# Kernel optimization log

Hardware: AMD Instinct MI355X
Metric: run time of the kernel (lower is better)

## Reference

```python
import jax, jax.numpy as jnp
import numpy as np

INPUT_SIZE = 2048
OUTPUT_SIZE = 2048
BATCH = 8192


def setup_inputs() -> dict:
    key = jax.random.key(0)
    ks = jax.random.split(key, 11)
    in_dim = INPUT_SIZE + OUTPUT_SIZE
    bound = 1.0 / np.sqrt(in_dim)  # torch nn.Linear default init range
    def lin(kw, kb):
        W = jax.random.uniform(kw, (OUTPUT_SIZE, in_dim), jnp.float32, -bound, bound)
        b = jax.random.uniform(kb, (OUTPUT_SIZE,), jnp.float32, -bound, bound)
        return W, b
    W1, b1 = lin(ks[0], ks[1])
    W2, b2 = lin(ks[2], ks[3])
    W3, b3 = lin(ks[4], ks[5])
    W4, b4 = lin(ks[6], ks[7])
    i = jax.random.normal(ks[8], (BATCH, INPUT_SIZE), jnp.float32)
    h = jax.random.normal(ks[9], (BATCH, OUTPUT_SIZE), jnp.float32)
    c = jax.random.normal(ks[10], (BATCH, OUTPUT_SIZE), jnp.float32)
    return {"i": i, "h": h, "c": c,
            "W1": W1, "b1": b1, "W2": W2, "b2": b2,
            "W3": W3, "b3": b3, "W4": W4, "b4": b4}


def reference(i, h, c, W1, b1, W2, b2, W3, b3, W4, b4):
    ih = jnp.concatenate((i, h), axis=1)  # [B, input+output]
    o1 = jax.nn.sigmoid(ih @ W1.T + b1)   # forget gate
    o2 = jax.nn.sigmoid(ih @ W2.T + b2)   # input gate
    o3 = jnp.tanh(ih @ W3.T + b3)         # candidate
    o4 = jax.nn.sigmoid(ih @ W4.T + b4)   # output gate
    new_c = c * o1 + o2 * o3
    # NOTE: faithful to the source: new_h uses tanh of the OLD cell state c
    new_h = jnp.tanh(c) * o4
    return (new_h, new_c)
```

## Files before the change

### kernel.cpp

```cpp
#include <hip/hip_runtime.h>
#include <hip/hip_bf16.h>
#include <stdint.h>

#define GLOBAL_AS __attribute__((address_space(1)))
#define LDS_AS    __attribute__((address_space(3)))

typedef __attribute__((ext_vector_type(8))) short  short8;
typedef __attribute__((ext_vector_type(4))) float  floatx4;

constexpr int BATCH = 8192;
constexpr int OUT   = 2048;
constexpr int KDIM  = 4096;

constexpr size_t IH_ELEMS = (size_t)BATCH * KDIM;
constexpr size_t W_ELEMS  = (size_t)4 * OUT * KDIM;

constexpr int TBM = 256;
constexpr int TBN = 256;
constexpr int TBK = 64;
constexpr int TNT = KDIM / TBK;

__device__ __forceinline__ unsigned int cvt2(float a, float b) {
    union { __hip_bfloat162 h; unsigned int u; } v;
    v.h = __float22bfloat162_rn(make_float2(a, b));
    return v.u;
}
__device__ __forceinline__ float sigmoidf_(float x) {
    return 1.0f / (1.0f + __expf(-x));
}
__device__ __forceinline__ void stage16(const unsigned short* g, unsigned short* l) {
    __builtin_amdgcn_global_load_lds((const GLOBAL_AS uint32_t*)g,
                                     (LDS_AS uint32_t*)l, 16, 0, 0);
}
__device__ __forceinline__ floatx4 mfma16(short8 a, short8 b, floatx4 c) {
    return __builtin_amdgcn_mfma_f32_16x16x32_bf16(a, b, c, 0, 0, 0);
}


__global__ __launch_bounds__(256)
void cvt_all(const float* __restrict__ I, const float* __restrict__ H,
             const float* __restrict__ W1, const float* __restrict__ W2,
             const float* __restrict__ W3, const float* __restrict__ W4,
             unsigned short* __restrict__ dst)
{
    const size_t t = (size_t)blockIdx.x * 256 + threadIdx.x;
    const size_t e = t * 8;
    const float* s;
    if (e < IH_ELEMS) {
        const int b = (int)(e >> 12);
        const int k = (int)(e & 4095);
        s = (k < 2048) ? (I + (size_t)b * 2048 + k)
                       : (H + (size_t)b * 2048 + (k - 2048));
    } else {
        const size_t e2 = e - IH_ELEMS;
        const int g = (int)(e2 >> 23);
        const size_t rem = e2 & 8388607u;
        const float* Wg = (g == 0) ? W1 : (g == 1) ? W2 : (g == 2) ? W3 : W4;
        s = Wg + rem;
    }
    const float4 x = ((const float4*)s)[0];
    const float4 y = ((const float4*)s)[1];
    uint4 o;
    o.x = cvt2(x.x, x.y); o.y = cvt2(x.z, x.w);
    o.z = cvt2(y.x, y.y); o.w = cvt2(y.z, y.w);
    *(uint4*)(dst + e) = o;
}


__global__ __launch_bounds__(512, 2)
void lstm_gemm_8ph(const unsigned short* __restrict__ ihb,
                   const unsigned short* __restrict__ Wb,
                   const float* __restrict__ C,
                   const float* __restrict__ B1, const float* __restrict__ B2,
                   const float* __restrict__ B3, const float* __restrict__ B4,
                   float* __restrict__ Outp)
{
    __shared__ unsigned short smem[65536];

    const int tid  = threadIdx.x;
    const int w    = tid >> 6;
    const int lane = tid & 63;
    const int col  = lane & 15;
    const int q    = lane >> 4;
    const int wr   = w >> 2;
    const int wc   = w & 3;

    const int bid = blockIdx.x;
    const int swz = (bid & 7) * 128 + (bid >> 3);
    const int bx  = swz & 31;
    const int by  = swz >> 5;
    const int bm0 = by * TBM;
    const int o0  = bx * 64;

    const unsigned short* srcA[2];
    const unsigned short* srcB[2];
    #pragma unroll
    for (int j = 0; j < 2; ++j) {
        const int c  = (w * 2 + j) * 64 + lane;
        const int r  = c >> 3;
        const int s  = c & 7;
        const int kc = s ^ (r & 7);
        srcA[j] = ihb + (size_t)(bm0 + r) * KDIM + kc * 8;
        const int g  = (r >> 4) & 3;
        const int oo = o0 + (r >> 6) * 16 + (r & 15);
        srcB[j] = Wb + (size_t)(g * OUT + oo) * KDIM + kc * 8;
    }
    const int sliceA = w * 1024;

    const int c7    = col & 7;
    const int slot0 = ((0 + q) ^ c7) * 8;
    const int slot1 = ((4 + q) ^ c7) * 8;
    const int aBase = wr * 8192 + col * 64;
    const int bBase = 16384 + (wc >> 1) * 8192 + ((wc & 1) * 64 + col) * 64;

    floatx4 acc[8][4];
    #pragma unroll
    for (int i = 0; i < 8; ++i)
        #pragma unroll
        for (int j = 0; j < 4; ++j)
            acc[i][j] = (floatx4){0.f, 0.f, 0.f, 0.f};

    stage16(srcA[0],                  &smem[0     + sliceA]);
    stage16(srcA[1],                  &smem[0     + sliceA + 512]);
    stage16(srcA[0] + 128 * KDIM,     &smem[8192  + sliceA]);
    stage16(srcA[1] + 128 * KDIM,     &smem[8192  + sliceA + 512]);
    stage16(srcB[0],                  &smem[16384 + sliceA]);
    stage16(srcB[1],                  &smem[16384 + sliceA + 512]);
    stage16(srcB[0] + 32 * KDIM,      &smem[24576 + sliceA]);
    stage16(srcB[1] + 32 * KDIM,      &smem[24576 + sliceA + 512]);
    stage16(srcB[0] + TBK,            &smem[32768 + 16384 + sliceA]);
    stage16(srcB[1] + TBK,            &smem[32768 + 16384 + sliceA + 512]);
    stage16(srcB[0] + 32 * KDIM + TBK, &smem[32768 + 24576 + sliceA]);
    stage16(srcB[1] + 32 * KDIM + TBK, &smem[32768 + 24576 + sliceA + 512]);
    asm volatile("s_waitcnt vmcnt(4)" ::: "memory");
    __builtin_amdgcn_s_barrier();

    short8 Af[4][2];
    short8 Bf[2][2][2];

    for (int t = 0; t < TNT; ++t) {
        const int buf = t & 1;
        const unsigned short* Ab = smem + buf * 32768 + aBase;
        const unsigned short* Bb = smem + buf * 32768 + bBase;
        unsigned short* stA = smem + (buf ^ 1) * 32768;
        unsigned short* stB = smem + buf * 32768;
        const int kA = ((t + 1) < TNT ? (t + 1) : TNT - 1) * TBK;
        const int kB = ((t + 2) < TNT ? (t + 2) : TNT - 1) * TBK;

        #pragma unroll
        for (int tm = 0; tm < 4; ++tm) {
            Af[tm][0] = *(const short8*)(Ab + tm * 1024 + slot0);
            Af[tm][1] = *(const short8*)(Ab + tm * 1024 + slot1);
        }
        #pragma unroll
        for (int tn = 0; tn < 2; ++tn) {
            Bf[0][tn][0] = *(const short8*)(Bb + tn * 1024 + slot0);
            Bf[0][tn][1] = *(const short8*)(Bb + tn * 1024 + slot1);
        }
        stage16(srcA[0] + kA, stA + 0 + sliceA);
        stage16(srcA[1] + kA, stA + 0 + sliceA + 512);
        __builtin_amdgcn_s_barrier();
        asm volatile("s_waitcnt lgkmcnt(0)" ::: "memory");
        __builtin_amdgcn_sched_barrier(0);
        __builtin_amdgcn_s_setprio(1);
        #pragma unroll
        for (int tm = 0; tm < 4; ++tm)
            #pragma unroll
            for (int tn = 0; tn < 2; ++tn) {
                acc[tm][tn] = mfma16(Af[tm][0], Bf[0][tn][0], acc[tm][tn]);
                acc[tm][tn] = mfma16(Af[tm][1], Bf[0][tn][1], acc[tm][tn]);
            }
        __builtin_amdgcn_s_setprio(0);
        __builtin_amdgcn_s_barrier();

        #pragma unroll
        for (int tn = 0; tn < 2; ++tn) {
            Bf[1][tn][0] = *(const short8*)(Bb + 2048 + tn * 1024 + slot0);
            Bf[1][tn][1] = *(const short8*)(Bb + 2048 + tn * 1024 + slot1);
        }
        stage16(srcA[0] + 128 * KDIM + kA, stA + 8192 + sliceA);
        stage16(srcA[1] + 128 * KDIM + kA, stA + 8192 + sliceA + 512);
        __builtin_amdgcn_s_barrier();
        asm volatile("s_waitcnt lgkmcnt(0)" ::: "memory");
        __builtin_amdgcn_sched_barrier(0);
        __builtin_amdgcn_s_setprio(1);
        #pragma unroll
        for (int tm = 0; tm < 4; ++tm)
            #pragma unroll
            for (int tn = 0; tn < 2; ++tn) {
                acc[tm][2 + tn] = mfma16(Af[tm][0], Bf[1][tn][0], acc[tm][2 + tn]);
                acc[tm][2 + tn] = mfma16(Af[tm][1], Bf[1][tn][1], acc[tm][2 + tn]);
            }
        __builtin_amdgcn_s_setprio(0);
        __builtin_amdgcn_s_barrier();

        #pragma unroll
        for (int tm = 0; tm < 4; ++tm) {
            Af[tm][0] = *(const short8*)(Ab + 4096 + tm * 1024 + slot0);
            Af[tm][1] = *(const short8*)(Ab + 4096 + tm * 1024 + slot1);
        }
        stage16(srcB[0] + kB, stB + 16384 + sliceA);
        stage16(srcB[1] + kB, stB + 16384 + sliceA + 512);
        __builtin_amdgcn_s_barrier();
        asm volatile("s_waitcnt lgkmcnt(0)" ::: "memory");
        __builtin_amdgcn_sched_barrier(0);
        __builtin_amdgcn_s_setprio(1);
        #pragma unroll
        for (int tm = 0; tm < 4; ++tm)
            #pragma unroll
            for (int tn = 0; tn < 2; ++tn) {
                acc[4 + tm][tn] = mfma16(Af[tm][0], Bf[0][tn][0], acc[4 + tm][tn]);
                acc[4 + tm][tn] = mfma16(Af[tm][1], Bf[0][tn][1], acc[4 + tm][tn]);
            }
        __builtin_amdgcn_s_setprio(0);
        __builtin_amdgcn_s_barrier();

        stage16(srcB[0] + 32 * KDIM + kB, stB + 24576 + sliceA);
        stage16(srcB[1] + 32 * KDIM + kB, stB + 24576 + sliceA + 512);
        __builtin_amdgcn_s_barrier();
        asm volatile("s_waitcnt lgkmcnt(0)" ::: "memory");
        __builtin_amdgcn_sched_barrier(0);
        __builtin_amdgcn_s_setprio(1);
        #pragma unroll
        for (int tm = 0; tm < 4; ++tm)
            #pragma unroll
            for (int tn = 0; tn < 2; ++tn) {
                acc[4 + tm][2 + tn] = mfma16(Af[tm][0], Bf[1][tn][0], acc[4 + tm][2 + tn]);
                acc[4 + tm][2 + tn] = mfma16(Af[tm][1], Bf[1][tn][1], acc[4 + tm][2 + tn]);
            }
        __builtin_amdgcn_s_setprio(0);
        asm volatile("s_waitcnt vmcnt(4)" ::: "memory");
        __builtin_amdgcn_s_barrier();
    }

    const int o = o0 + wc * 16 + col;
    float bias[4];
    bias[0] = B1[o]; bias[1] = B2[o]; bias[2] = B3[o]; bias[3] = B4[o];

    const size_t HALF = (size_t)BATCH * OUT;
    #pragma unroll
    for (int tm = 0; tm < 8; ++tm) {
        #pragma unroll
        for (int r = 0; r < 4; ++r) {
            const int b = bm0 + wr * 128 + tm * 16 + q * 4 + r;
            const size_t idx = (size_t)b * OUT + o;
            const float cv = C[idx];
            const float o1 = sigmoidf_(acc[tm][0][r] + bias[0]);
            const float o2 = sigmoidf_(acc[tm][1][r] + bias[1]);
            const float o3 = tanhf    (acc[tm][2][r] + bias[2]);
            const float o4 = sigmoidf_(acc[tm][3][r] + bias[3]);
            Outp[idx]        = tanhf(cv) * o4;
            Outp[HALF + idx] = cv * o1 + o2 * o3;
        }
    }
}


constexpr int FBM = 128;
constexpr int FBO = 32;
constexpr int FBK = 32;

__global__ __launch_bounds__(256)
void lstm_fused_f32(const float* __restrict__ I, const float* __restrict__ H,
                    const float* __restrict__ C,
                    const float* __restrict__ W1, const float* __restrict__ B1,
                    const float* __restrict__ W2, const float* __restrict__ B2,
                    const float* __restrict__ W3, const float* __restrict__ B3,
                    const float* __restrict__ W4, const float* __restrict__ B4,
                    float* __restrict__ Outp)
{
    __shared__ unsigned short As[FBM * FBK];
    __shared__ unsigned short Bs[4 * FBO * FBK];

    const int tid  = threadIdx.x;
    const int w    = tid >> 6;
    const int lane = tid & 63;
    const int col  = lane & 15;
    const int q    = lane >> 4;

    const int bm0 = blockIdx.y * FBM;
    const int o0  = blockIdx.x * FBO;

    long aoff[2], boff[2];
    const float* wptr[2];
    unsigned short* dstA[2];
    unsigned short* dstB[2];
    #pragma unroll
    for (int j = 0; j < 2; ++j) {
        const int win = w * 2 + j;
        const int c   = win * 64 + lane;
        const int row = c >> 2;
        const int kcs = c & 3;
        const int kc  = kcs ^ ((row >> 1) & 3);
        aoff[j] = (long)(bm0 + row) * (KDIM / 2) + kc * 8;
        const int g = row >> 5;
        const int o = o0 + (row & 31);
        wptr[j] = (g == 0) ? W1 : (g == 1) ? W2 : (g == 2) ? W3 : W4;
        boff[j] = (long)o * KDIM + kc * 8;
        dstA[j] = As + (size_t)c * 8;
        dstB[j] = Bs + (size_t)c * 8;
    }

    int aAddr[2];
    #pragma unroll
    for (int tm = 0; tm < 2; ++tm) {
        const int m = w * 32 + tm * 16 + col;
        aAddr[tm] = (m * 4 + (q ^ ((m >> 1) & 3))) * 8;
    }
    int bAddr[8];
    #pragma unroll
    for (int tn = 0; tn < 8; ++tn) {
        const int n = tn * 16 + col;
        bAddr[tn] = (n * 4 + (q ^ ((n >> 1) & 3))) * 8;
    }

    floatx4 acc[2][8];
    #pragma unroll
    for (int tm = 0; tm < 2; ++tm)
        #pragma unroll
        for (int tn = 0; tn < 8; ++tn)
            acc[tm][tn] = (floatx4){0.f, 0.f, 0.f, 0.f};

    for (int k0 = 0; k0 < KDIM; k0 += FBK) {
        #pragma unroll
        for (int j = 0; j < 2; ++j) {
            const float* ab = (k0 < KDIM / 2) ? (I + k0) : (H + (k0 - KDIM / 2));
            const float* sa = ab + aoff[j];
            const float* sb = wptr[j] + boff[j] + k0;
            const float4 a0 = ((const float4*)sa)[0];
            const float4 a1 = ((const float4*)sa)[1];
            const float4 b0 = ((const float4*)sb)[0];
            const float4 b1 = ((const float4*)sb)[1];
            uint4 va, vb;
            va.x = cvt2(a0.x, a0.y); va.y = cvt2(a0.z, a0.w);
            va.z = cvt2(a1.x, a1.y); va.w = cvt2(a1.z, a1.w);
            vb.x = cvt2(b0.x, b0.y); vb.y = cvt2(b0.z, b0.w);
            vb.z = cvt2(b1.x, b1.y); vb.w = cvt2(b1.z, b1.w);
            *(uint4*)dstA[j] = va;
            *(uint4*)dstB[j] = vb;
        }
        __syncthreads();

        const short8 a0 = *(const short8*)(As + aAddr[0]);
        const short8 a1 = *(const short8*)(As + aAddr[1]);
        #pragma unroll
        for (int tn = 0; tn < 8; ++tn) {
            const short8 b = *(const short8*)(Bs + bAddr[tn]);
            acc[0][tn] = __builtin_amdgcn_mfma_f32_16x16x32_bf16(a0, b, acc[0][tn], 0, 0, 0);
            acc[1][tn] = __builtin_amdgcn_mfma_f32_16x16x32_bf16(a1, b, acc[1][tn], 0, 0, 0);
        }
        __syncthreads();
    }

    float bias[2][4];
    #pragma unroll
    for (int obit = 0; obit < 2; ++obit) {
        const int o = o0 + obit * 16 + col;
        bias[obit][0] = B1[o]; bias[obit][1] = B2[o];
        bias[obit][2] = B3[o]; bias[obit][3] = B4[o];
    }

    const size_t HALF = (size_t)BATCH * OUT;
    #pragma unroll
    for (int tm = 0; tm < 2; ++tm) {
        #pragma unroll
        for (int r = 0; r < 4; ++r) {
            const int b = bm0 + w * 32 + tm * 16 + q * 4 + r;
            #pragma unroll
            for (int obit = 0; obit < 2; ++obit) {
                const int o = o0 + obit * 16 + col;
                const size_t idx = (size_t)b * OUT + o;
                const float cv = C[idx];
                const float o1 = sigmoidf_(acc[tm][0 + obit][r] + bias[obit][0]);
                const float o2 = sigmoidf_(acc[tm][2 + obit][r] + bias[obit][1]);
                const float o3 = tanhf   (acc[tm][4 + obit][r] + bias[obit][2]);
                const float o4 = sigmoidf_(acc[tm][6 + obit][r] + bias[obit][3]);
                Outp[idx]        = tanhf(cv) * o4;
                Outp[HALF + idx] = cv * o1 + o2 * o3;
            }
        }
    }
}

extern "C" void kernel_launch(void* const* d_in, const int* in_sizes, int n_in,
                              void* d_out, int out_size, void* d_ws, size_t ws_size,
                              hipStream_t stream) {
    const float* I  = (const float*)d_in[0];
    const float* H  = (const float*)d_in[1];
    const float* C  = (const float*)d_in[2];
    const float* W1 = (const float*)d_in[3];
    const float* B1 = (const float*)d_in[4];
    const float* W2 = (const float*)d_in[5];
    const float* B2 = (const float*)d_in[6];
    const float* W3 = (const float*)d_in[7];
    const float* B3 = (const float*)d_in[8];
    const float* W4 = (const float*)d_in[9];
    const float* B4 = (const float*)d_in[10];
    float* Outp = (float*)d_out;

    const size_t need = (IH_ELEMS + W_ELEMS) * 2;

    if (ws_size >= need) {
        unsigned short* ihb = (unsigned short*)d_ws;
        unsigned short* Wb  = ihb + IH_ELEMS;
        const int cvt_blocks = (int)((IH_ELEMS + W_ELEMS) / 8 / 256);
        cvt_all<<<cvt_blocks, 256, 0, stream>>>(I, H, W1, W2, W3, W4, ihb);
        lstm_gemm_8ph<<<dim3((BATCH / TBM) * (OUT / (TBN / 4))), dim3(512), 0, stream>>>(
            ihb, Wb, C, B1, B2, B3, B4, Outp);
    } else {
        dim3 grid(OUT / FBO, BATCH / FBM);
        lstm_fused_f32<<<grid, 256, 0, stream>>>(I, H, C, W1, B1, W2, B2,
                                                 W3, B3, W4, B4, Outp);
    }
}
```

Baseline: 837.1 us.

## Software-pipeline LDS fragment loads one phase ahead of MFMA clusters

Restructures the main K loop so each MFMA cluster consumes fragments loaded during the previous phase. A second A-fragment register set lets the second half's A data and the next tile's A/B fragments be prefetched from LDS while the current MFMAs run. Global-to-LDS staging moves to after the MFMA clusters, and the explicit lgkmcnt(0) waits before each cluster are removed. This raises register pressure and reshuffles barriers and vmcnt waits, which risks LDS race hazards or a loss of occupancy.

Measured after the change: 841.7 us. Within noise of the previous version (+0.6%).

```diff
diff --git a/kernel.cpp b/kernel.cpp
--- a/kernel.cpp
+++ b/kernel.cpp
@@ -120,47 +120,57 @@
         for (int j = 0; j < 4; ++j)
             acc[i][j] = (floatx4){0.f, 0.f, 0.f, 0.f};
 
-    stage16(srcA[0],                  &smem[0     + sliceA]);
-    stage16(srcA[1],                  &smem[0     + sliceA + 512]);
-    stage16(srcA[0] + 128 * KDIM,     &smem[8192  + sliceA]);
-    stage16(srcA[1] + 128 * KDIM,     &smem[8192  + sliceA + 512]);
-    stage16(srcB[0],                  &smem[16384 + sliceA]);
-    stage16(srcB[1],                  &smem[16384 + sliceA + 512]);
-    stage16(srcB[0] + 32 * KDIM,      &smem[24576 + sliceA]);
-    stage16(srcB[1] + 32 * KDIM,      &smem[24576 + sliceA + 512]);
-    stage16(srcB[0] + TBK,            &smem[32768 + 16384 + sliceA]);
-    stage16(srcB[1] + TBK,            &smem[32768 + 16384 + sliceA + 512]);
+    stage16(srcA[0],                   &smem[0     + sliceA]);
+    stage16(srcA[1],                   &smem[0     + sliceA + 512]);
+    stage16(srcA[0] + 128 * KDIM,      &smem[8192  + sliceA]);
+    stage16(srcA[1] + 128 * KDIM,      &smem[8192  + sliceA + 512]);
+    stage16(srcB[0],                   &smem[16384 + sliceA]);
+    stage16(srcB[1],                   &smem[16384 + sliceA + 512]);
+    stage16(srcB[0] + 32 * KDIM,       &smem[24576 + sliceA]);
+    stage16(srcB[1] + 32 * KDIM,       &smem[24576 + sliceA + 512]);
+    stage16(srcB[0] + TBK,             &smem[32768 + 16384 + sliceA]);
+    stage16(srcB[1] + TBK,             &smem[32768 + 16384 + sliceA + 512]);
     stage16(srcB[0] + 32 * KDIM + TBK, &smem[32768 + 24576 + sliceA]);
     stage16(srcB[1] + 32 * KDIM + TBK, &smem[32768 + 24576 + sliceA + 512]);
     asm volatile("s_waitcnt vmcnt(4)" ::: "memory");
     __builtin_amdgcn_s_barrier();
 
     short8 Af[4][2];
+    short8 Af2[4][2];
     short8 Bf[2][2][2];
+
+    {
+        const unsigned short* Ab0 = smem + aBase;
+        const unsigned short* Bb0 = smem + bBase;
+        #pragma unroll
+        for (int tm = 0; tm < 4; ++tm) {
+            Af[tm][0] = *(const short8*)(Ab0 + tm * 1024 + slot0);
+            Af[tm][1] = *(const short8*)(Ab0 + tm * 1024 + slot1);
+        }
+        #pragma unroll
+        for (int tn = 0; tn < 2; ++tn) {
+            Bf[0][tn][0] = *(const short8*)(Bb0 + tn * 1024 + slot0);
+            Bf[0][tn][1] = *(const short8*)(Bb0 + tn * 1024 + slot1);
+        }
+    }
 
     for (int t = 0; t < TNT; ++t) {
         const int buf = t & 1;
-        const unsigned short* Ab = smem + buf * 32768 + aBase;
-        const unsigned short* Bb = smem + buf * 32768 + bBase;
+        const unsigned short* Ab  = smem + buf * 32768 + aBase;
+        const unsigned short* Bb  = smem + buf * 32768 + bBase;
+        const unsigned short* Abn = smem + (buf ^ 1) * 32768 + aBase;
+        const unsigned short* Bbn = smem + (buf ^ 1) * 32768 + bBase;
         unsigned short* stA = smem + (buf ^ 1) * 32768;
         unsigned short* stB = smem + buf * 32768;
         const int kA = ((t + 1) < TNT ? (t + 1) : TNT - 1) * TBK;
         const int kB = ((t + 2) < TNT ? (t + 2) : TNT - 1) * TBK;
 
-        #pragma unroll
-        for (int tm = 0; tm < 4; ++tm) {
-            Af[tm][0] = *(const short8*)(Ab + tm * 1024 + slot0);
-            Af[tm][1] = *(const short8*)(Ab + tm * 1024 + slot1);
-        }
+        __builtin_amdgcn_s_barrier();
         #pragma unroll
         for (int tn = 0; tn < 2; ++tn) {
-            Bf[0][tn][0] = *(const short8*)(Bb + tn * 1024 + slot0);
-            Bf[0][tn][1] = *(const short8*)(Bb + tn * 1024 + slot1);
-        }
-        stage16(srcA[0] + kA, stA + 0 + sliceA);
-        stage16(srcA[1] + kA, stA + 0 + sliceA + 512);
-        __builtin_amdgcn_s_barrier();
-        asm volatile("s_waitcnt lgkmcnt(0)" ::: "memory");
+            Bf[1][tn][0] = *(const short8*)(Bb + 2048 + tn * 1024 + slot0);
+            Bf[1][tn][1] = *(const short8*)(Bb + 2048 + tn * 1024 + slot1);
+        }
         __builtin_amdgcn_sched_barrier(0);
         __builtin_amdgcn_s_setprio(1);
         #pragma unroll
@@ -171,17 +181,17 @@
                 acc[tm][tn] = mfma16(Af[tm][1], Bf[0][tn][1], acc[tm][tn]);
             }
         __builtin_amdgcn_s_setprio(0);
-        __builtin_amdgcn_s_barrier();
-
-        #pragma unroll
-        for (int tn = 0; tn < 2; ++tn) {
-            Bf[1][tn][0] = *(const short8*)(Bb + 2048 + tn * 1024 + slot0);
-            Bf[1][tn][1] = *(const short8*)(Bb + 2048 + tn * 1024 + slot1);
-        }
+        stage16(srcA[0] + kA,             stA + 0    + sliceA);
+        stage16(srcA[1] + kA,             stA + 0    + sliceA + 512);
         stage16(srcA[0] + 128 * KDIM + kA, stA + 8192 + sliceA);
         stage16(srcA[1] + 128 * KDIM + kA, stA + 8192 + sliceA + 512);
+
         __builtin_amdgcn_s_barrier();
-        asm volatile("s_waitcnt lgkmcnt(0)" ::: "memory");
+        #pragma unroll
+        for (int tm = 0; tm < 4; ++tm) {
+            Af2[tm][0] = *(const short8*)(Ab + 4096 + tm * 1024 + slot0);
+            Af2[tm][1] = *(const short8*)(Ab + 4096 + tm * 1024 + slot1);
+        }
         __builtin_amdgcn_sched_barrier(0);
         __builtin_amdgcn_s_setprio(1);
         #pragma unroll
@@ -192,45 +202,45 @@
                 acc[tm][2 + tn] = mfma16(Af[tm][1], Bf[1][tn][1], acc[tm][2 + tn]);
             }
         __builtin_amdgcn_s_setprio(0);
+
         __builtin_amdgcn_s_barrier();
-
-        #pragma unroll
-        for (int tm = 0; tm < 4; ++tm) {
-            Af[tm][0] = *(const short8*)(Ab + 4096 + tm * 1024 + slot0);
-            Af[tm][1] = *(const short8*)(Ab + 4096 + tm * 1024 + slot1);
-        }
-        stage16(srcB[0] + kB, stB + 16384 + sliceA);
-        stage16(srcB[1] + kB, stB + 16384 + sliceA + 512);
-        __builtin_amdgcn_s_barrier();
-        asm volatile("s_waitcnt lgkmcnt(0)" ::: "memory");
         __builtin_amdgcn_sched_barrier(0);
         __builtin_amdgcn_s_setprio(1);
         #pragma unroll
         for (int tm = 0; tm < 4; ++tm)
             #pragma unroll
             for (int tn = 0; tn < 2; ++tn) {
-                acc[4 + tm][tn] = mfma16(Af[tm][0], Bf[0][tn][0], acc[4 + tm][tn]);
-                acc[4 + tm][tn] = mfma16(Af[tm][1], Bf[0][tn][1], acc[4 + tm][tn]);
+                acc[4 + tm][tn] = mfma16(Af2[tm][0], Bf[0][tn][0], acc[4 + tm][tn]);
+                acc[4 + tm][tn] = mfma16(Af2[tm][1], Bf[0][tn][1], acc[4 + tm][tn]);
             }
         __builtin_amdgcn_s_setprio(0);
+        stage16(srcB[0] + kB, stB + 16384 + sliceA);
+        stage16(srcB[1] + kB, stB + 16384 + sliceA + 512);
+
+        asm volatile("s_waitcnt vmcnt(2)" ::: "memory");
         __builtin_amdgcn_s_barrier();
-
-        stage16(srcB[0] + 32 * KDIM + kB, stB + 24576 + sliceA);
-        stage16(srcB[1] + 32 * KDIM + kB, stB + 24576 + sliceA + 512);
-        __builtin_amdgcn_s_barrier();
-        asm volatile("s_waitcnt lgkmcnt(0)" ::: "memory");
+        #pragma unroll
+        for (int tm = 0; tm < 4; ++tm) {
+            Af[tm][0] = *(const short8*)(Abn + tm * 1024 + slot0);
+            Af[tm][1] = *(const short8*)(Abn + tm * 1024 + slot1);
+        }
+        #pragma unroll
+        for (int tn = 0; tn < 2; ++tn) {
+            Bf[0][tn][0] = *(const short8*)(Bbn + tn * 1024 + slot0);
+            Bf[0][tn][1] = *(const short8*)(Bbn + tn * 1024 + slot1);
+        }
         __builtin_amdgcn_sched_barrier(0);
         __builtin_amdgcn_s_setprio(1);
         #pragma unroll
         for (int tm = 0; tm < 4; ++tm)
             #pragma unroll
             for (int tn = 0; tn < 2; ++tn) {
-                acc[4 + tm][2 + tn] = mfma16(Af[tm][0], Bf[1][tn][0], acc[4 + tm][2 + tn]);
-                acc[4 + tm][2 + tn] = mfma16(Af[tm][1], Bf[1][tn][1], acc[4 + tm][2 + tn]);
+                acc[4 + tm][2 + tn] = mfma16(Af2[tm][0], Bf[1][tn][0], acc[4 + tm][2 + tn]);
+                acc[4 + tm][2 + tn] = mfma16(Af2[tm][1], Bf[1][tn][1], acc[4 + tm][2 + tn]);
             }
         __builtin_amdgcn_s_setprio(0);
-        asm volatile("s_waitcnt vmcnt(4)" ::: "memory");
-        __builtin_amdgcn_s_barrier();
+        stage16(srcB[0] + 32 * KDIM + kB, stB + 24576 + sliceA);
+        stage16(srcB[1] + 32 * KDIM + kB, stB + 24576 + sliceA + 512);
     }
 
     const int o = o0 + wc * 16 + col;
```
